# Kernel tuning notes

Hardware: AMD Instinct MI355X
Metric: run time of the kernel (lower is better)

Reference implementation:

```python
import jax, jax.numpy as jnp
import numpy as np

BLOCK_SIZE = 32
BITS = 4
Q_MAX = 2 ** (BITS - 1) - 1  # 7


def setup_inputs() -> dict:
    key = jax.random.key(0)
    k1, k2, k3, k4 = jax.random.split(key, 4)
    B, S, D_in, D_out = 4, 2048, 4096, 4096
    x = jax.random.normal(k1, (B, S, D_in), dtype=jnp.float32)
    # 4-bit symmetric quantized values in [-8, 7], stored as int32
    weight_q = jax.random.randint(k2, (D_out, D_in), -(2 ** (BITS - 1)), 2 ** (BITS - 1), dtype=jnp.int32)
    # per-block positive scales (abs-max of each block in the original)
    block_scales = jax.random.uniform(k3, (D_out, D_in // BLOCK_SIZE), dtype=jnp.float32, minval=0.01, maxval=1.0)
    bias = jax.random.normal(k4, (D_out,), dtype=jnp.float32) * 0.01
    return {"x": x, "weight_q": weight_q, "block_scales": block_scales, "bias": bias}


def _dequantize(weight_q, block_scales):
    out_f, in_f = weight_q.shape
    n_blocks = in_f // BLOCK_SIZE
    q = weight_q.reshape(out_f, n_blocks, BLOCK_SIZE).astype(jnp.float32)
    w = q / Q_MAX * block_scales[:, :, None]
    return w.reshape(out_f, in_f)


def reference(x, weight_q, block_scales, bias):
    # block dequantize: w = q / q_max * scale, then y = x @ w.T + b
    w = _dequantize(weight_q, block_scales)  # [out, in] fp32
    return jnp.einsum('bsi,oi->bso', x, w) + bias
```

## Files before the change

### kernel.cpp

```cpp
#include <hip/hip_runtime.h>
#include <stdint.h>

#define M_DIM 8192
#define N_DIM 4096
#define K_DIM 4096
#define NBLK  (K_DIM / 32)

typedef __attribute__((ext_vector_type(4))) float          f32x4;
typedef __attribute__((ext_vector_type(8))) short          bf16x8;
typedef __attribute__((ext_vector_type(4))) int            i32x4;
typedef __attribute__((ext_vector_type(8))) unsigned short u16x8;
typedef __attribute__((address_space(3))) unsigned short   lds_us;

__device__ __forceinline__ unsigned short f2bf(float f) {
  unsigned u = __builtin_bit_cast(unsigned, f);
  u += 0x7fffu + ((u >> 16) & 1u);
  return (unsigned short)(u >> 16);
}

__device__ __forceinline__ void stage16(const unsigned short* g, lds_us* l) {
  __builtin_amdgcn_global_load_lds(
      (const __attribute__((address_space(1))) void*)g,
      (__attribute__((address_space(3))) void*)l, 16, 0, 0);
}

template <int OFF>
__device__ __forceinline__ bf16x8 dsr(lds_us* addr) {
  bf16x8 d;
  asm volatile("ds_read_b128 %0, %1 offset:%2" : "=v"(d) : "v"(addr), "n"(OFF));
  return d;
}


__global__ void MXFP4_dequant_kernel(const int* __restrict__ wq,
                                     const float* __restrict__ scales,
                                     unsigned short* __restrict__ wb) {
  size_t t = (size_t)blockIdx.x * 256 + threadIdx.x;
  int slot = (int)(t & 63);
  int r = slot & 15, c = slot >> 4;
  int sub = (int)(t >> 6) & 15;
  int R = sub >> 1, Kt = sub & 1;
  int H = (int)(t >> 10) & 31;
  int g = (int)(t >> 15);
  size_t row = (size_t)H * 128 + R * 16 + r;
  size_t k   = (size_t)g * 64 + Kt * 32 + c * 8;
  float s = scales[row * NBLK + (g * 2 + Kt)] * (1.0f / 7.0f);
  const int* src = wq + row * K_DIM + k;
  i32x4 q0 = *(const i32x4*)src;
  i32x4 q1 = *(const i32x4*)(src + 4);
  u16x8 out;
#pragma unroll
  for (int j = 0; j < 4; ++j) out[j]     = f2bf((float)q0[j] * s);
#pragma unroll
  for (int j = 0; j < 4; ++j) out[4 + j] = f2bf((float)q1[j] * s);
  *(u16x8*)(wb + t * 8) = out;
}

__global__ void MXFP4_cvt_kernel(const float* __restrict__ x,
                                 unsigned short* __restrict__ xb) {
  size_t t = (size_t)blockIdx.x * 256 + threadIdx.x;
  int slot = (int)(t & 63);
  int r = slot & 15, c = slot >> 4;
  int sub = (int)(t >> 6) & 15;
  int R = sub >> 1, Kt = sub & 1;
  int H = (int)(t >> 10) & 63;
  int g = (int)(t >> 16);
  size_t row = (size_t)H * 128 + R * 16 + r;
  size_t k   = (size_t)g * 64 + Kt * 32 + c * 8;
  const float* src = x + row * K_DIM + k;
  f32x4 v0 = *(const f32x4*)src;
  f32x4 v1 = *(const f32x4*)(src + 4);
  u16x8 out;
#pragma unroll
  for (int j = 0; j < 4; ++j) out[j]     = f2bf(v0[j]);
#pragma unroll
  for (int j = 0; j < 4; ++j) out[4 + j] = f2bf(v1[j]);
  *(u16x8*)(xb + t * 8) = out;
}


#define BAR() __builtin_amdgcn_s_barrier()
#define WAIT_LGKM(N_) do { asm volatile("s_waitcnt lgkmcnt(%0)" :: "n"(N_) : "memory"); \
                           __builtin_amdgcn_sched_barrier(0); } while (0)

#define ST_A(t_, h_, BUFA_, valid_) do { \
  if (valid_) { \
    const unsigned short* s_ = Abase + ((size_t)(t_) * 64 + (h_)) * 8192 + tid8; \
    lds_us* d_ = lp + (BUFA_) * 16384 + (h_) * 8192 + tid8; \
    stage16(s_, d_); stage16(s_ + 4096, d_ + 4096); \
  } else { stage16(Abase + tid8, lp + 65536); \
           stage16(Abase + tid8 + 4096, lp + 65536 + 512); } \
} while (0)

#define ST_B(t_, h_, BUFB_, valid_) do { \
  if (valid_) { \
    const unsigned short* s_ = Bbase + ((size_t)(t_) * 32 + (h_)) * 8192 + tid8; \
    lds_us* d_ = lp + 32768 + (BUFB_) * 16384 + (h_) * 8192 + tid8; \
    stage16(s_, d_); stage16(s_ + 4096, d_ + 4096); \
  } else { stage16(Bbase + tid8, lp + 65536); \
           stage16(Bbase + tid8 + 4096, lp + 65536 + 512); } \
} while (0)

#define MF(MB_, NB_, AF_, BF_) do { \
  _Pragma("unroll") \
  for (int kk_ = 0; kk_ < 2; ++kk_) \
    _Pragma("unroll") \
    for (int mm_ = 0; mm_ < 4; ++mm_) \
      _Pragma("unroll") \
      for (int nn_ = 0; nn_ < 2; ++nn_) \
        acc[(MB_) + mm_][(NB_) + nn_] = __builtin_amdgcn_mfma_f32_16x16x32_bf16( \
            AF_[mm_][kk_], BF_[nn_][kk_], acc[(MB_) + mm_][(NB_) + nn_], 0, 0, 0); \
} while (0)

#define RD_ALO_BLO(dsA_, dsB_) do { \
  aLo[0][0] = dsr<0>(dsA_);      aLo[0][1] = dsr<1024>(dsA_); \
  aLo[1][0] = dsr<2048>(dsA_);   aLo[1][1] = dsr<3072>(dsA_); \
  aLo[2][0] = dsr<4096>(dsA_);   aLo[2][1] = dsr<5120>(dsA_); \
  aLo[3][0] = dsr<6144>(dsA_);   aLo[3][1] = dsr<7168>(dsA_); \
  bLo[0][0] = dsr<0>(dsB_);      bLo[0][1] = dsr<1024>(dsB_); \
  bLo[1][0] = dsr<2048>(dsB_);   bLo[1][1] = dsr<3072>(dsB_); \
} while (0)

#define GROUP(BUF_, tB_, tA_, vB_, vA_, RDN_) do { \
  lds_us* dsA_ = lp + (BUF_) * 16384 + wm * 8192 + lane * 8; \
  lds_us* dsB_ = lp + 32768 + (BUF_) * 16384 + wn * 4096 + lane * 8; \
  lds_us* dsA2_ = lp + ((BUF_) ^ 1) * 16384 + wm * 8192 + lane * 8; \
  lds_us* dsB2_ = lp + 32768 + ((BUF_) ^ 1) * 16384 + wn * 4096 + lane * 8; \
   \
  aHi[0][0] = dsr<8192>(dsA_);   aHi[0][1] = dsr<9216>(dsA_); \
  aHi[1][0] = dsr<10240>(dsA_);  aHi[1][1] = dsr<11264>(dsA_); \
  aHi[2][0] = dsr<12288>(dsA_);  aHi[2][1] = dsr<13312>(dsA_); \
  aHi[3][0] = dsr<14336>(dsA_);  aHi[3][1] = dsr<15360>(dsA_); \
  ST_B(tB_, 0, (BUF_) ^ 1, vB_); \
  BAR(); WAIT_LGKM(8);  \
  __builtin_amdgcn_s_setprio(1); \
  MF(0, 0, aLo, bLo); \
  __builtin_amdgcn_s_setprio(0); \
  BAR(); \
   \
  bHi[0][0] = dsr<4096>(dsB_);   bHi[0][1] = dsr<5120>(dsB_); \
  bHi[1][0] = dsr<6144>(dsB_);   bHi[1][1] = dsr<7168>(dsB_); \
  ST_B(tB_, 1, (BUF_) ^ 1, vB_); \
  BAR(); WAIT_LGKM(4);  \
  __builtin_amdgcn_s_setprio(1); \
  MF(4, 0, aHi, bLo); \
  __builtin_amdgcn_s_setprio(0); \
  BAR(); \
   \
  ST_A(tA_, 0, (BUF_), vA_); \
  BAR(); WAIT_LGKM(0);  \
  __builtin_amdgcn_s_setprio(1); \
  MF(0, 2, aLo, bHi); \
  __builtin_amdgcn_s_setprio(0); \
  BAR(); \
   \
  ST_A(tA_, 1, (BUF_), vA_); \
  asm volatile("s_waitcnt vmcnt(4)" ::: "memory"); \
  BAR(); \
  if (RDN_) { RD_ALO_BLO(dsA2_, dsB2_); } \
  __builtin_amdgcn_s_setprio(1); \
  MF(4, 2, aHi, bHi); \
  __builtin_amdgcn_s_setprio(0); \
  BAR(); \
} while (0)

__global__ __launch_bounds__(512, 2) void MXFP4_gemm_kernel(
    const unsigned short* __restrict__ A,
    const unsigned short* __restrict__ B,
    const float* __restrict__ bias,
    float* __restrict__ C) {
  __shared__ unsigned short LDS[66560];
  lds_us* lp = (lds_us*)LDS;

  const int tid  = threadIdx.x;
  const int lane = tid & 63;
  const int wv   = tid >> 6;
  const int wm   = wv >> 2;
  const int wn   = wv & 3;
  const int tid8 = tid * 8;

  const int bid = blockIdx.x;
  const int xcd = bid & 7;
  const int idx = bid >> 3;
  const int tm  = (xcd & 3) * 8 + (idx & 7);
  const int tn  = (xcd >> 2) * 8 + (idx >> 3);
  const int brow = tm * 256;
  const int bcol = tn * 256;

  const unsigned short* Abase = A + (size_t)(tm * 2) * 8192;
  const unsigned short* Bbase = B + (size_t)(tn * 2) * 8192;

  f32x4 acc[8][4] = {};
  bf16x8 aLo[4][2], aHi[4][2], bLo[2][2], bHi[2][2];

  ST_A(0, 0, 0, true); ST_A(0, 1, 0, true);
  ST_B(0, 0, 0, true); ST_B(0, 1, 0, true);
  ST_A(1, 0, 1, true); ST_A(1, 1, 1, true);
  asm volatile("s_waitcnt vmcnt(4)" ::: "memory");
  BAR();
  {
    lds_us* dsA0 = lp + wm * 8192 + lane * 8;
    lds_us* dsB0 = lp + 32768 + wn * 4096 + lane * 8;
    RD_ALO_BLO(dsA0, dsB0);
  }

  for (int it = 0; it < 31; ++it) {
    const int g0 = 2 * it;
    GROUP(0, g0 + 1, g0 + 2, true, true, true);
    GROUP(1, g0 + 2, g0 + 3, true, true, true);
  }
  GROUP(0, 63, 64, true, false, true);
  GROUP(1, 64, 65, false, false, false);

  const int rb = brow + wm * 128 + (lane >> 4) * 4;
  const int cb = bcol + wn * 64 + (lane & 15);
#pragma unroll
  for (int n = 0; n < 4; ++n) {
    const int col = cb + n * 16;
    const float bv = bias[col];
#pragma unroll
    for (int m = 0; m < 8; ++m) {
      const int row = rb + m * 16;
#pragma unroll
      for (int j = 0; j < 4; ++j)
        C[(size_t)(row + j) * N_DIM + col] = acc[m][n][j] + bv;
    }
  }
}

extern "C" void kernel_launch(void* const* d_in, const int* in_sizes, int n_in,
                              void* d_out, int out_size, void* d_ws, size_t ws_size,
                              hipStream_t stream) {
  const float* x      = (const float*)d_in[0];
  const int*   wq     = (const int*)d_in[1];
  const float* scales = (const float*)d_in[2];
  const float* bias   = (const float*)d_in[3];
  float*       out    = (float*)d_out;

  unsigned short* wb = (unsigned short*)d_ws;
  unsigned short* xb = wb + (size_t)N_DIM * K_DIM;

  MXFP4_dequant_kernel<<<(N_DIM * (long)K_DIM / 8) / 256, 256, 0, stream>>>(wq, scales, wb);
  MXFP4_cvt_kernel<<<(M_DIM * (long)K_DIM / 8) / 256, 256, 0, stream>>>(x, xb);

  MXFP4_gemm_kernel<<<512, 512, 0, stream>>>(xb, wb, bias, out);
}
```

Before: 305.0 us.

## Switch GEMM to 32x32x16 bf16 MFMA with matching pre-swizzled operand layouts

Replaces the 16x16x32 bf16 MFMA tiling with 32x32x16 MFMA instructions, so each wave issues fewer, larger matrix ops per K step. The dequant and convert kernels are rewritten to emit operands in the fragment layout the 32x32 instruction expects, and the epilogue row/column mapping is changed to match the 32x32 accumulator layout. The aim is fewer MFMA issues and better operand reuse per LDS read. The cost is a different accumulator register layout, and the existing barrier and wait schedule must still line up with the new instruction latencies.

```diff
diff --git a/kernel.cpp b/kernel.cpp
--- a/kernel.cpp
+++ b/kernel.cpp
@@ -6,11 +6,12 @@
 #define K_DIM 4096
 #define NBLK  (K_DIM / 32)
 
-typedef __attribute__((ext_vector_type(4))) float          f32x4;
-typedef __attribute__((ext_vector_type(8))) short          bf16x8;
-typedef __attribute__((ext_vector_type(4))) int            i32x4;
-typedef __attribute__((ext_vector_type(8))) unsigned short u16x8;
-typedef __attribute__((address_space(3))) unsigned short   lds_us;
+typedef __attribute__((ext_vector_type(4)))  float          f32x4;
+typedef __attribute__((ext_vector_type(16))) float          f32x16;
+typedef __attribute__((ext_vector_type(8)))  short          bf16x8;
+typedef __attribute__((ext_vector_type(4)))  int            i32x4;
+typedef __attribute__((ext_vector_type(8)))  unsigned short u16x8;
+typedef __attribute__((address_space(3)))    unsigned short lds_us;
 
 __device__ __forceinline__ unsigned short f2bf(float f) {
   unsigned u = __builtin_bit_cast(unsigned, f);
@@ -36,15 +37,15 @@
                                      const float* __restrict__ scales,
                                      unsigned short* __restrict__ wb) {
   size_t t = (size_t)blockIdx.x * 256 + threadIdx.x;
-  int slot = (int)(t & 63);
-  int r = slot & 15, c = slot >> 4;
+  int l  = (int)(t & 63);
+  int r  = l & 31, cq = l >> 5;
   int sub = (int)(t >> 6) & 15;
-  int R = sub >> 1, Kt = sub & 1;
+  int mb = sub >> 2, ks = sub & 3;
   int H = (int)(t >> 10) & 31;
   int g = (int)(t >> 15);
-  size_t row = (size_t)H * 128 + R * 16 + r;
-  size_t k   = (size_t)g * 64 + Kt * 32 + c * 8;
-  float s = scales[row * NBLK + (g * 2 + Kt)] * (1.0f / 7.0f);
+  size_t row = (size_t)H * 128 + mb * 32 + r;
+  size_t k   = (size_t)g * 64 + ks * 16 + cq * 8;
+  float s = scales[row * NBLK + (k >> 5)] * (1.0f / 7.0f);
   const int* src = wq + row * K_DIM + k;
   i32x4 q0 = *(const i32x4*)src;
   i32x4 q1 = *(const i32x4*)(src + 4);
@@ -59,14 +60,14 @@
 __global__ void MXFP4_cvt_kernel(const float* __restrict__ x,
                                  unsigned short* __restrict__ xb) {
   size_t t = (size_t)blockIdx.x * 256 + threadIdx.x;
-  int slot = (int)(t & 63);
-  int r = slot & 15, c = slot >> 4;
+  int l  = (int)(t & 63);
+  int r  = l & 31, cq = l >> 5;
   int sub = (int)(t >> 6) & 15;
-  int R = sub >> 1, Kt = sub & 1;
+  int mb = sub >> 2, ks = sub & 3;
   int H = (int)(t >> 10) & 63;
   int g = (int)(t >> 16);
-  size_t row = (size_t)H * 128 + R * 16 + r;
-  size_t k   = (size_t)g * 64 + Kt * 32 + c * 8;
+  size_t row = (size_t)H * 128 + mb * 32 + r;
+  size_t k   = (size_t)g * 64 + ks * 16 + cq * 8;
   const float* src = x + row * K_DIM + k;
   f32x4 v0 = *(const f32x4*)src;
   f32x4 v1 = *(const f32x4*)(src + 4);
@@ -103,22 +104,20 @@
 
 #define MF(MB_, NB_, AF_, BF_) do { \
   _Pragma("unroll") \
-  for (int kk_ = 0; kk_ < 2; ++kk_) \
+  for (int ks_ = 0; ks_ < 4; ++ks_) \
     _Pragma("unroll") \
-    for (int mm_ = 0; mm_ < 4; ++mm_) \
-      _Pragma("unroll") \
-      for (int nn_ = 0; nn_ < 2; ++nn_) \
-        acc[(MB_) + mm_][(NB_) + nn_] = __builtin_amdgcn_mfma_f32_16x16x32_bf16( \
-            AF_[mm_][kk_], BF_[nn_][kk_], acc[(MB_) + mm_][(NB_) + nn_], 0, 0, 0); \
+    for (int mm_ = 0; mm_ < 2; ++mm_) \
+      acc[(MB_) + mm_][NB_] = __builtin_amdgcn_mfma_f32_32x32x16_bf16( \
+          AF_[mm_][ks_], BF_[ks_], acc[(MB_) + mm_][NB_], 0, 0, 0); \
 } while (0)
 
 #define RD_ALO_BLO(dsA_, dsB_) do { \
   aLo[0][0] = dsr<0>(dsA_);      aLo[0][1] = dsr<1024>(dsA_); \
-  aLo[1][0] = dsr<2048>(dsA_);   aLo[1][1] = dsr<3072>(dsA_); \
-  aLo[2][0] = dsr<4096>(dsA_);   aLo[2][1] = dsr<5120>(dsA_); \
-  aLo[3][0] = dsr<6144>(dsA_);   aLo[3][1] = dsr<7168>(dsA_); \
-  bLo[0][0] = dsr<0>(dsB_);      bLo[0][1] = dsr<1024>(dsB_); \
-  bLo[1][0] = dsr<2048>(dsB_);   bLo[1][1] = dsr<3072>(dsB_); \
+  aLo[0][2] = dsr<2048>(dsA_);   aLo[0][3] = dsr<3072>(dsA_); \
+  aLo[1][0] = dsr<4096>(dsA_);   aLo[1][1] = dsr<5120>(dsA_); \
+  aLo[1][2] = dsr<6144>(dsA_);   aLo[1][3] = dsr<7168>(dsA_); \
+  bLo[0] = dsr<0>(dsB_);         bLo[1] = dsr<1024>(dsB_); \
+  bLo[2] = dsr<2048>(dsB_);      bLo[3] = dsr<3072>(dsB_); \
 } while (0)
 
 #define GROUP(BUF_, tB_, tA_, vB_, vA_, RDN_) do { \
@@ -128,9 +127,9 @@
   lds_us* dsB2_ = lp + 32768 + ((BUF_) ^ 1) * 16384 + wn * 4096 + lane * 8; \
    \
   aHi[0][0] = dsr<8192>(dsA_);   aHi[0][1] = dsr<9216>(dsA_); \
-  aHi[1][0] = dsr<10240>(dsA_);  aHi[1][1] = dsr<11264>(dsA_); \
-  aHi[2][0] = dsr<12288>(dsA_);  aHi[2][1] = dsr<13312>(dsA_); \
-  aHi[3][0] = dsr<14336>(dsA_);  aHi[3][1] = dsr<15360>(dsA_); \
+  aHi[0][2] = dsr<10240>(dsA_);  aHi[0][3] = dsr<11264>(dsA_); \
+  aHi[1][0] = dsr<12288>(dsA_);  aHi[1][1] = dsr<13312>(dsA_); \
+  aHi[1][2] = dsr<14336>(dsA_);  aHi[1][3] = dsr<15360>(dsA_); \
   ST_B(tB_, 0, (BUF_) ^ 1, vB_); \
   BAR(); WAIT_LGKM(8);  \
   __builtin_amdgcn_s_setprio(1); \
@@ -138,19 +137,19 @@
   __builtin_amdgcn_s_setprio(0); \
   BAR(); \
    \
-  bHi[0][0] = dsr<4096>(dsB_);   bHi[0][1] = dsr<5120>(dsB_); \
-  bHi[1][0] = dsr<6144>(dsB_);   bHi[1][1] = dsr<7168>(dsB_); \
+  bHi[0] = dsr<4096>(dsB_);      bHi[1] = dsr<5120>(dsB_); \
+  bHi[2] = dsr<6144>(dsB_);      bHi[3] = dsr<7168>(dsB_); \
   ST_B(tB_, 1, (BUF_) ^ 1, vB_); \
   BAR(); WAIT_LGKM(4);  \
   __builtin_amdgcn_s_setprio(1); \
-  MF(4, 0, aHi, bLo); \
+  MF(2, 0, aHi, bLo); \
   __builtin_amdgcn_s_setprio(0); \
   BAR(); \
    \
   ST_A(tA_, 0, (BUF_), vA_); \
   BAR(); WAIT_LGKM(0);  \
   __builtin_amdgcn_s_setprio(1); \
-  MF(0, 2, aLo, bHi); \
+  MF(0, 1, aLo, bHi); \
   __builtin_amdgcn_s_setprio(0); \
   BAR(); \
    \
@@ -159,7 +158,7 @@
   BAR(); \
   if (RDN_) { RD_ALO_BLO(dsA2_, dsB2_); } \
   __builtin_amdgcn_s_setprio(1); \
-  MF(4, 2, aHi, bHi); \
+  MF(2, 1, aHi, bHi); \
   __builtin_amdgcn_s_setprio(0); \
   BAR(); \
 } while (0)
@@ -190,8 +189,8 @@
   const unsigned short* Abase = A + (size_t)(tm * 2) * 8192;
   const unsigned short* Bbase = B + (size_t)(tn * 2) * 8192;
 
-  f32x4 acc[8][4] = {};
-  bf16x8 aLo[4][2], aHi[4][2], bLo[2][2], bHi[2][2];
+  f32x16 acc[4][2] = {};
+  bf16x8 aLo[2][4], aHi[2][4], bLo[4], bHi[4];
 
   ST_A(0, 0, 0, true); ST_A(0, 1, 0, true);
   ST_B(0, 0, 0, true); ST_B(0, 1, 0, true);
@@ -212,18 +211,20 @@
   GROUP(0, 63, 64, true, false, true);
   GROUP(1, 64, 65, false, false, false);
 
-  const int rb = brow + wm * 128 + (lane >> 4) * 4;
-  const int cb = bcol + wn * 64 + (lane & 15);
-#pragma unroll
-  for (int n = 0; n < 4; ++n) {
-    const int col = cb + n * 16;
+  const int rb = brow + wm * 128 + 4 * (lane >> 5);
+  const int cb = bcol + wn * 64 + (lane & 31);
+#pragma unroll
+  for (int nb = 0; nb < 2; ++nb) {
+    const int col = cb + nb * 32;
     const float bv = bias[col];
 #pragma unroll
-    for (int m = 0; m < 8; ++m) {
-      const int row = rb + m * 16;
-#pragma unroll
-      for (int j = 0; j < 4; ++j)
-        C[(size_t)(row + j) * N_DIM + col] = acc[m][n][j] + bv;
+    for (int mb = 0; mb < 4; ++mb) {
+      const int rowb = rb + mb * 32;
+#pragma unroll
+      for (int rg = 0; rg < 16; ++rg) {
+        const int row = rowb + (rg & 3) + 8 * (rg >> 2);
+        C[(size_t)row * N_DIM + col] = acc[mb][nb][rg] + bv;
+      }
     }
   }
 }
```

Result: slower. 312.5 us (+2.5%).
